# Kernel tuning notes

Measured on AMD Instinct MI355X. Metric: run time of the kernel, lower is better.

Reference implementation:

```python
import jax, jax.numpy as jnp
import numpy as np

B = 1024
IN_SIZ = 16384
OUT_SIZ = 16384
C = 8          # channel_siz
NLVL = 10
IFS = IN_SIZ // 2 ** NLVL                                   # 16, in_filter_siz
KLVL = min(int(np.floor(np.log2(OUT_SIZ / 2))), NLVL)       # 10
OFS = OUT_SIZ // 2 ** KLVL                                  # 16, out_filter_siz
STD = 0.9


def setup_inputs() -> dict:
    key = jax.random.key(0)
    ks = jax.random.split(key, 2 * NLVL + 3)
    inp = {}
    inp["x"] = jax.random.normal(ks[0], (B, IN_SIZ, 1), jnp.float32)
    inp["in_filter"] = jax.random.normal(ks[1], (IFS, 1, C), jnp.float32) * STD
    inp["in_bias"] = jnp.zeros((C,), jnp.float32)
    for lvl in range(1, NLVL + 1):
        k = 2 ** lvl
        inp[f"W{lvl}"] = jax.random.normal(ks[2 * lvl], (k, 2, C, C), jnp.float32) * STD
        inp[f"b{lvl}"] = jnp.zeros((k, C), jnp.float32)
    inp["fea_dense"] = jax.random.normal(ks[-1], (2 ** KLVL, C, OFS), jnp.float32) * STD
    return inp


def _level(v, W, b):
    # v: [Kp, B, L, C] parent branches; W: [2*Kp, 2, C, C]; b: [2*Kp, C]
    # kernel-2 stride-2 conv1d: out[t] = relu(x[2t] @ W[0] + x[2t+1] @ W[1] + b)
    Kp, Bn, L, Cc = v.shape
    xp = v.reshape(Kp, Bn, L // 2, 2, Cc)
    xr = jnp.repeat(xp, 2, axis=0)  # child itk reads parent itk // 2
    y = jnp.einsum('kbtsc,kscd->kbtd', xr, W) + b[:, None, None, :]
    return jax.nn.relu(y)


def reference(x, in_filter, in_bias,
              W1, b1, W2, b2, W3, b3, W4, b4, W5, b5,
              W6, b6, W7, b7, W8, b8, W9, b9, W10, b10,
              fea_dense):
    Ws = [W1, W2, W3, W4, W5, W6, W7, W8, W9, W10]
    bs = [b1, b2, b3, b4, b5, b6, b7, b8, b9, b10]
    Bn = x.shape[0]
    # input conv1d: kernel=IFS, stride=IFS (non-overlapping) == blocked matmul
    xin = x[..., 0].reshape(Bn, 2 ** NLVL, IFS)                       # [B, 1024, 16]
    v = jax.nn.relu(jnp.einsum('bnf,fc->bnc', xin, in_filter[:, 0, :]) + in_bias)
    v = v[None]                                                        # [1, B, 1024, C]
    for lvl in range(NLVL):  # klvl == nlvl: all levels branch (tree doubling)
        v = _level(v, Ws[lvl], bs[lvl])
    # v: [2^klvl, B, 1, C] -> per-branch dense feature map
    out = jnp.einsum('kbc,kcf->bkf', v[:, :, 0, :], fea_dense)         # [B, 1024, OFS]
    return out.reshape(Bn, OUT_SIZ, 1)
```

## Files before the change

kernel.cpp:

```cpp
#include <hip/hip_runtime.h>

struct PrepPtrs {
  const float* W[7]; const float* Bv[7]; const float* F; const float* fb;
  const float* W8; const float* B8; const float* W9; const float* B9;
  const float* W10; const float* B10;
};

__device__ __forceinline__ int cz(int c) { return c ^ ((c >> 3) & 3); }

__device__ __forceinline__ float4 relu4(float4 a) {
  return make_float4(fmaxf(a.x,0.f), fmaxf(a.y,0.f), fmaxf(a.z,0.f), fmaxf(a.w,0.f));
}
__device__ __forceinline__ void fma4(float4& acc, float s, const float4& wv) {
  acc.x = fmaf(s, wv.x, acc.x); acc.y = fmaf(s, wv.y, acc.y);
  acc.z = fmaf(s, wv.z, acc.z); acc.w = fmaf(s, wv.w, acc.w);
}
__device__ __forceinline__ float4 add4(float4 a, float4 b) {
  return make_float4(a.x+b.x, a.y+b.y, a.z+b.z, a.w+b.w);
}

__device__ __forceinline__ float4 entApply(const float4* __restrict__ e4,
                                           float4 A0, float4 A1,
                                           float4 C0, float4 C1) {
  float4 a0 = e4[16];
  float4 a1 = make_float4(0.f, 0.f, 0.f, 0.f);
  float4 a2 = make_float4(0.f, 0.f, 0.f, 0.f);
  float4 a3 = make_float4(0.f, 0.f, 0.f, 0.f);
  fma4(a0, A0.x, e4[0]);  fma4(a1, A0.y, e4[1]);  fma4(a2, A0.z, e4[2]);  fma4(a3, A0.w, e4[3]);
  fma4(a0, A1.x, e4[4]);  fma4(a1, A1.y, e4[5]);  fma4(a2, A1.z, e4[6]);  fma4(a3, A1.w, e4[7]);
  fma4(a0, C0.x, e4[8]);  fma4(a1, C0.y, e4[9]);  fma4(a2, C0.z, e4[10]); fma4(a3, C0.w, e4[11]);
  fma4(a0, C1.x, e4[12]); fma4(a1, C1.y, e4[13]); fma4(a2, C1.z, e4[14]); fma4(a3, C1.w, e4[15]);
  return relu4(add4(add4(a0, a1), add4(a2, a3)));
}

__global__ void bfly_prep(PrepPtrs P, float* __restrict__ wt) {
  int e = blockIdx.x * 256 + threadIdx.x;
  if (e >= 4094 * 68) return;
  int ent = e / 68, r = e % 68, dd = r & 3;
  const float* Ws; const float* Bs; int th;
  if (ent < 62) {
    if (ent < 60) {
      int lvl, base;
      if (ent < 4)       { lvl = 1; base = 0;  }
      else if (ent < 12) { lvl = 2; base = 4;  }
      else if (ent < 28) { lvl = 3; base = 12; }
      else               { lvl = 4; base = 28; }
      int k = (ent - base) >> 1; th = ent & 1;
      Ws = P.W[lvl-1] + k*128; Bs = P.Bv[lvl-1] + k*8;
    } else {
      th = ent - 60; Ws = P.F; Bs = P.fb;
    }
  } else if (ent < 510) {
    int eb = ent - 62;
    int q = eb / 56, rem = eb % 56;
    int lvl, Kl, base;
    if (rem < 8)       { lvl = 5; Kl = 4;  base = 0;  }
    else if (rem < 24) { lvl = 6; Kl = 8;  base = 8;  }
    else               { lvl = 7; Kl = 16; base = 24; }
    int rr = rem - base; int lk = rr >> 1; th = rr & 1;
    int kg = q * Kl + lk;
    Ws = P.W[lvl-1] + kg*128; Bs = P.Bv[lvl-1] + kg*8;
  } else if (ent < 1022) {
    int ec = ent - 510; int k = ec >> 1; th = ec & 1;
    Ws = P.W8 + k*128; Bs = P.B8 + k*8;
  } else if (ent < 2046) {
    int ec = ent - 1022; int k = ec >> 1; th = ec & 1;
    Ws = P.W9 + k*128; Bs = P.B9 + k*8;
  } else {
    int ec = ent - 2046; int k = ec >> 1; th = ec & 1;
    Ws = P.W10 + k*128; Bs = P.B10 + k*8;
  }
  float v;
  if (r < 64) { int s = r >> 5, c = (r >> 2) & 7; v = Ws[s*64 + c*8 + th*4 + dd]; }
  else v = Bs[th*4 + dd];
  wt[ent * 80 + r] = v;
}

template<int L>
__device__ __forceinline__ void ka_level(const float4* __restrict__ src,
                                         float4* __restrict__ dst,
                                         const float4* __restrict__ wt4,
                                         int lane, int wq, int th) {
  constexpr int Kc = 1 << L, Tc = 1024 >> L;
  constexpr int entBase = (Kc - 2) * 2;
  constexpr int kIters = (L <= 2) ? 1 : (1 << (L - 2));
  constexpr int tIters = 4 / kIters;
#pragma unroll
  for (int ik = 0; ik < kIters; ++ik) {
    int k;
    if constexpr (L == 1) k = wq & 1;
    else if constexpr (L == 2) k = wq;
    else k = wq + 4 * ik;
    const float4* e4 = wt4 + (entBase + k * 2 + th) * 20;
    const int kp = k >> 1;
#pragma unroll
    for (int it = 0; it < tIters; ++it) {
      int t;
      if constexpr (L == 1) t = lane + (wq >> 1) * 64 + it * 128;
      else if constexpr (L == 2) t = lane + it * 64;
      else if constexpr (L == 3) t = lane + it * 64;
      else t = lane;
      int pb = kp * (2 * Tc) + 2 * t;
      float4 A0 = src[cz(pb)],        C0 = src[cz(pb + 1)];
      float4 A1 = src[cz(pb + 1024)], C1 = src[cz(pb + 1025)];
      dst[cz(th * 1024 + k * Tc + t)] = entApply(e4, A0, A1, C0, C1);
    }
  }
}

__global__ __launch_bounds__(512, 2) void bfly_ka(
    const float* __restrict__ x, const float* __restrict__ wt,
    float* __restrict__ st1)
{
  __shared__ float4 sA[2048], sB[2048];
  const int tid = threadIdx.x, b = blockIdx.x;
  const int lane = tid & 63;
  const int wv = __builtin_amdgcn_readfirstlane(tid >> 6);
  const int th = wv & 1, wq = wv >> 1;
  const float4* wt4 = (const float4*)wt;

  {
    const float4* e4 = wt4 + (60 + th) * 20;
    const float* xb = x + (size_t)b * 16384;
#pragma unroll
    for (int i = 0; i < 4; ++i) {
      int n = lane + wq * 64 + i * 256;
      const float4* xr = (const float4*)(xb + n * 16);
      float4 x0 = xr[0], x1 = xr[1], x2 = xr[2], x3 = xr[3];
      sA[cz(th * 1024 + n)] = entApply(e4, x0, x1, x2, x3);
    }
  }
  __syncthreads();
  ka_level<1>(sA, sB, wt4, lane, wq, th); __syncthreads();
  ka_level<2>(sB, sA, wt4, lane, wq, th); __syncthreads();
  ka_level<3>(sA, sB, wt4, lane, wq, th); __syncthreads();
  ka_level<4>(sB, sA, wt4, lane, wq, th); __syncthreads();

  float4* o4 = (float4*)st1;
#pragma unroll
  for (int it = 0; it < 4; ++it) {
    int o = tid + it * 512;
    int t4 = o & 63, k4 = (o >> 6) & 15, h = o >> 10;
    o4[((size_t)(h * 16 + k4) * 1024 + b) * 64 + t4] = sA[cz(o)];
  }
}

template<int LV>
__device__ __forceinline__ void kb_level(const float4* __restrict__ src,
                                         float4* __restrict__ dst,
                                         const float4* __restrict__ wb4,
                                         int lane, int wv) {
  constexpr int Kc = 1 << (LV - 3);
  constexpr int Tc = 128 / Kc;
  constexpr int Tp = 256 / Kc;
  constexpr int entB = (LV == 5) ? 0 : (LV == 6) ? 8 : 24;
  constexpr int kIters = Kc / 4;
  constexpr int nIt = 4 / kIters;
  const int th = wv & 1, w2 = wv >> 1;
#pragma unroll
  for (int ik = 0; ik < kIters; ++ik) {
    const int lk = w2 + 4 * ik;
    const float4* e4 = wb4 + (entB + lk * 2 + th) * 20;
    const int lkp = lk >> 1;
#pragma unroll
    for (int it = 0; it < nIt; ++it) {
      int t, bb;
      if constexpr (LV == 5)      { t = lane & 31; bb = (lane >> 5) + it * 2; }
      else if constexpr (LV == 6) { t = lane & 15; bb = (lane >> 4) + it * 4; }
      else                        { t = lane & 7;  bb = lane >> 3; }
      int pb = bb * 256 + lkp * Tp + 2 * t;
      float4 A0 = src[cz(pb)],       C0 = src[cz(pb + 1)];
      float4 A1 = src[cz(pb + 128)], C1 = src[cz(pb + 129)];
      dst[cz(bb * 256 + th * 128 + lk * Tc + t)] = entApply(e4, A0, A1, C0, C1);
    }
  }
}

__global__ __launch_bounds__(512, 2) void bfly_kb(
    const float* __restrict__ st1, const float* __restrict__ wt,
    float* __restrict__ st2)
{
  __shared__ float4 s0[2048], s1[2048];
  const int tid = threadIdx.x;
  const int q = blockIdx.x, bt = blockIdx.y;
  const int lane = tid & 63;
  const int wv = __builtin_amdgcn_readfirstlane(tid >> 6);
  const float4* wb4 = (const float4*)wt + 1240 + q * 56 * 20;
  const float4* i4 = (const float4*)st1;

#pragma unroll
  for (int it = 0; it < 4; ++it) {
    int o = tid + it * 512;
    int t4 = o & 63, lk4 = (o >> 6) & 1, h = (o >> 7) & 1, bl = o >> 8;
    float4 v = i4[((size_t)(h * 16 + 2 * q + lk4) * 1024 + bt * 8 + bl) * 64 + t4];
    s0[cz(bl * 256 + h * 128 + lk4 * 64 + t4)] = v;
  }
  __syncthreads();
  kb_level<5>(s0, s1, wb4, lane, wv); __syncthreads();
  kb_level<6>(s1, s0, wb4, lane, wv); __syncthreads();
  kb_level<7>(s0, s1, wb4, lane, wv); __syncthreads();

  float4* o4 = (float4*)st2;
#pragma unroll
  for (int it = 0; it < 4; ++it) {
    int o = tid + it * 512;
    int bl = o & 7, t7 = (o >> 3) & 7, h = (o >> 6) & 1, lk7 = o >> 7;
    float4 v = s1[cz(bl * 256 + h * 128 + lk7 * 8 + t7)];
    o4[((size_t)((16 * q + lk7) * 8 + t7) * 2 + h) * 1024 + bt * 8 + bl] = v;
  }
}

__global__ __launch_bounds__(512, 2) void bfly_kc(
    const float* __restrict__ st, const float* __restrict__ wt,
    const float* __restrict__ fea, float* __restrict__ out)
{
  __shared__ float4 sA[1024], sB[1024];
  const int tid = threadIdx.x;
  const int j = blockIdx.x, b0 = blockIdx.y * 64;
  const int bb = tid & 63;
  const int w = __builtin_amdgcn_readfirstlane(tid >> 6);
  const float4* wt4 = (const float4*)wt;

  {
    const float4* s4 = (const float4*)st;
#pragma unroll
    for (int it = 0; it < 2; ++it) {
      int idx = tid + it * 512;
      int bl = idx & 63, h = (idx >> 6) & 1, t = idx >> 7;
      sA[h * 512 + t * 64 + bl] = s4[((size_t)((j * 8 + t) * 2 + h)) * 1024 + b0 + bl];
    }
  }
  __syncthreads();

#pragma unroll
  for (int ii = 0; ii < 2; ++ii) {
    int s = w + ii * 8;
    int th = s >> 3, k = (s >> 2) & 1, t = s & 3;
    const float4* e4 = wt4 + (510 + (2 * j + k) * 2 + th) * 20;
    float4 A0 = sA[(2*t) * 64 + bb],   A1 = sA[512 + (2*t) * 64 + bb];
    float4 C0 = sA[(2*t+1) * 64 + bb], C1 = sA[512 + (2*t+1) * 64 + bb];
    sB[th * 512 + (2*t + k) * 64 + bb] = entApply(e4, A0, A1, C0, C1);
  }
  __syncthreads();
#pragma unroll
  for (int ii = 0; ii < 2; ++ii) {
    int s = w + ii * 8;
    int th = s >> 3, k9 = (s >> 1) & 3, t9 = s & 1;
    const float4* e4 = wt4 + (1022 + (4 * j + k9) * 2 + th) * 20;
    int p0 = 4 * t9 + (k9 >> 1), p1 = p0 + 2;
    float4 A0 = sB[p0 * 64 + bb], A1 = sB[512 + p0 * 64 + bb];
    float4 C0 = sB[p1 * 64 + bb], C1 = sB[512 + p1 * 64 + bb];
    sA[th * 512 + (t9 * 4 + k9) * 64 + bb] = entApply(e4, A0, A1, C0, C1);
  }
  __syncthreads();
#pragma unroll
  for (int ii = 0; ii < 2; ++ii) {
    int s = w + ii * 8;
    int th = s >> 3, k10 = s & 7;
    const float4* e4 = wt4 + (2046 + (8 * j + k10) * 2 + th) * 20;
    int p0 = k10 >> 1, p1 = p0 + 4;
    float4 A0 = sA[p0 * 64 + bb], A1 = sA[512 + p0 * 64 + bb];
    float4 C0 = sA[p1 * 64 + bb], C1 = sA[512 + p1 * 64 + bb];
    sB[th * 512 + k10 * 64 + bb] = entApply(e4, A0, A1, C0, C1);
  }
  __syncthreads();
  {
    int cc = tid & 31, bgrp = tid >> 5;
    int k = cc >> 2, fq = cc & 3;
    const float* fp = fea + (size_t)(j * 8 + k) * 128 + fq * 4;
    float4 f0 = *(const float4*)(fp);        float4 f1 = *(const float4*)(fp + 16);
    float4 f2 = *(const float4*)(fp + 32);   float4 f3 = *(const float4*)(fp + 48);
    float4 f4_ = *(const float4*)(fp + 64);  float4 f5 = *(const float4*)(fp + 80);
    float4 f6 = *(const float4*)(fp + 96);   float4 f7 = *(const float4*)(fp + 112);
#pragma unroll
    for (int it = 0; it < 4; ++it) {
      int b_l = bgrp + it * 16;
      float4 s0v = sB[k * 64 + b_l];
      float4 s1v = sB[512 + k * 64 + b_l];
      float4 a0 = make_float4(0.f,0.f,0.f,0.f), a1 = make_float4(0.f,0.f,0.f,0.f);
      float4 a2 = make_float4(0.f,0.f,0.f,0.f), a3 = make_float4(0.f,0.f,0.f,0.f);
      fma4(a0, s0v.x, f0);  fma4(a1, s0v.y, f1);
      fma4(a2, s0v.z, f2);  fma4(a3, s0v.w, f3);
      fma4(a0, s1v.x, f4_); fma4(a1, s1v.y, f5);
      fma4(a2, s1v.z, f6);  fma4(a3, s1v.w, f7);
      float4 acc = add4(add4(a0, a1), add4(a2, a3));
      *(float4*)(out + ((size_t)(b0 + b_l)) * 16384 + j * 128 + k * 16 + fq * 4) = acc;
    }
  }
}

extern "C" void kernel_launch(void* const* d_in, const int* in_sizes, int n_in,
                              void* d_out, int out_size, void* d_ws, size_t ws_size,
                              hipStream_t stream) {
  const float* x  = (const float*)d_in[0];
  PrepPtrs P;
  P.F  = (const float*)d_in[1];
  P.fb = (const float*)d_in[2];
  for (int l = 0; l < 7; ++l) {
    P.W[l]  = (const float*)d_in[3 + 2 * l];
    P.Bv[l] = (const float*)d_in[4 + 2 * l];
  }
  P.W8  = (const float*)d_in[17];
  P.B8  = (const float*)d_in[18];
  P.W9  = (const float*)d_in[19];
  P.B9  = (const float*)d_in[20];
  P.W10 = (const float*)d_in[21];
  P.B10 = (const float*)d_in[22];
  const float* fea = (const float*)d_in[23];
  float* wt  = (float*)d_ws;
  float* st2 = (float*)d_ws + 393216;
  float* st1 = (float*)d_out;
  float* out = (float*)d_out;

  bfly_prep<<<dim3(1088), dim3(256), 0, stream>>>(P, wt);
  bfly_ka<<<dim3(1024), dim3(512), 0, stream>>>(x, wt, st1);
  bfly_kb<<<dim3(8, 128), dim3(512), 0, stream>>>(st1, wt, st2);
  bfly_kc<<<dim3(128, 16), dim3(512), 0, stream>>>(st2, wt, fea, out);
}
```

Baseline: 95.83 us.

## Compute all four children per thread from one parent load; make kb in-place

Each butterfly level now has a thread load its parent pair once into registers and produce all four child outputs (two child branches by two output halves), instead of reloading the same inputs for each child. This cuts shared-memory reads per level by about four times. bfly_kb now works in place in a single LDS buffer, which halves its shared memory and lets launch_bounds allow three blocks per CU. In-place updates are only safe because each (batch, parent) region is read and written by the same wavefront. The cost is higher register pressure, since each thread holds four outputs' worth of work.

```diff
diff --git a/kernel.cpp b/kernel.cpp
--- a/kernel.cpp
+++ b/kernel.cpp
@@ -77,35 +77,29 @@
 }
 
 template<int L>
-__device__ __forceinline__ void ka_level(const float4* __restrict__ src,
-                                         float4* __restrict__ dst,
-                                         const float4* __restrict__ wt4,
-                                         int lane, int wq, int th) {
-  constexpr int Kc = 1 << L, Tc = 1024 >> L;
-  constexpr int entBase = (Kc - 2) * 2;
-  constexpr int kIters = (L <= 2) ? 1 : (1 << (L - 2));
-  constexpr int tIters = 4 / kIters;
-#pragma unroll
-  for (int ik = 0; ik < kIters; ++ik) {
-    int k;
-    if constexpr (L == 1) k = wq & 1;
-    else if constexpr (L == 2) k = wq;
-    else k = wq + 4 * ik;
-    const float4* e4 = wt4 + (entBase + k * 2 + th) * 20;
-    const int kp = k >> 1;
-#pragma unroll
-    for (int it = 0; it < tIters; ++it) {
-      int t;
-      if constexpr (L == 1) t = lane + (wq >> 1) * 64 + it * 128;
-      else if constexpr (L == 2) t = lane + it * 64;
-      else if constexpr (L == 3) t = lane + it * 64;
-      else t = lane;
-      int pb = kp * (2 * Tc) + 2 * t;
-      float4 A0 = src[cz(pb)],        C0 = src[cz(pb + 1)];
-      float4 A1 = src[cz(pb + 1024)], C1 = src[cz(pb + 1025)];
-      dst[cz(th * 1024 + k * Tc + t)] = entApply(e4, A0, A1, C0, C1);
-    }
-  }
+__device__ __forceinline__ void ka_level2(const float4* __restrict__ src,
+                                          float4* __restrict__ dst,
+                                          const float4* __restrict__ wt4,
+                                          int lane, int w) {
+  constexpr int Tc = 1024 >> L;
+  constexpr int entBase = ((1 << L) - 2) * 2;
+  constexpr int TB = 1 << (4 - L);
+  const int kp = w >> (4 - L);
+  const int tb = w & (TB - 1);
+  const int t = lane + tb * 64;
+  const int pb = kp * (2 * Tc) + 2 * t;
+  const int cb = cz(pb);
+  const int cb1 = cb ^ 1;
+  float4 A0 = src[cb],        C0 = src[cb1];
+  float4 A1 = src[cb + 1024], C1 = src[cb1 + 1024];
+  float4* pD = dst + cz(2 * kp * Tc + t);
+#pragma unroll
+  for (int kk = 0; kk < 2; ++kk)
+#pragma unroll
+    for (int th = 0; th < 2; ++th) {
+      const float4* e4 = wt4 + (entBase + (2 * kp + kk) * 2 + th) * 20;
+      pD[kk * Tc + th * 1024] = entApply(e4, A0, A1, C0, C1);
+    }
 }
 
 __global__ __launch_bounds__(512, 2) void bfly_ka(
@@ -115,8 +109,8 @@
   __shared__ float4 sA[2048], sB[2048];
   const int tid = threadIdx.x, b = blockIdx.x;
   const int lane = tid & 63;
-  const int wv = __builtin_amdgcn_readfirstlane(tid >> 6);
-  const int th = wv & 1, wq = wv >> 1;
+  const int w = __builtin_amdgcn_readfirstlane(tid >> 6);
+  const int th = w & 1, wq = w >> 1;
   const float4* wt4 = (const float4*)wt;
 
   {
@@ -131,10 +125,10 @@
     }
   }
   __syncthreads();
-  ka_level<1>(sA, sB, wt4, lane, wq, th); __syncthreads();
-  ka_level<2>(sB, sA, wt4, lane, wq, th); __syncthreads();
-  ka_level<3>(sA, sB, wt4, lane, wq, th); __syncthreads();
-  ka_level<4>(sB, sA, wt4, lane, wq, th); __syncthreads();
+  ka_level2<1>(sA, sB, wt4, lane, w); __syncthreads();
+  ka_level2<2>(sB, sA, wt4, lane, w); __syncthreads();
+  ka_level2<3>(sA, sB, wt4, lane, w); __syncthreads();
+  ka_level2<4>(sB, sA, wt4, lane, w); __syncthreads();
 
   float4* o4 = (float4*)st1;
 #pragma unroll
@@ -146,45 +140,40 @@
 }
 
 template<int LV>
-__device__ __forceinline__ void kb_level(const float4* __restrict__ src,
-                                         float4* __restrict__ dst,
-                                         const float4* __restrict__ wb4,
-                                         int lane, int wv) {
-  constexpr int Kc = 1 << (LV - 3);
-  constexpr int Tc = 128 / Kc;
-  constexpr int Tp = 256 / Kc;
+__device__ __forceinline__ void kb_level2(float4* __restrict__ s,
+                                          const float4* __restrict__ wb4,
+                                          int lane, int w) {
+  constexpr int Tc = 1 << (10 - LV);
   constexpr int entB = (LV == 5) ? 0 : (LV == 6) ? 8 : 24;
-  constexpr int kIters = Kc / 4;
-  constexpr int nIt = 4 / kIters;
-  const int th = wv & 1, w2 = wv >> 1;
-#pragma unroll
-  for (int ik = 0; ik < kIters; ++ik) {
-    const int lk = w2 + 4 * ik;
-    const float4* e4 = wb4 + (entB + lk * 2 + th) * 20;
-    const int lkp = lk >> 1;
-#pragma unroll
-    for (int it = 0; it < nIt; ++it) {
-      int t, bb;
-      if constexpr (LV == 5)      { t = lane & 31; bb = (lane >> 5) + it * 2; }
-      else if constexpr (LV == 6) { t = lane & 15; bb = (lane >> 4) + it * 4; }
-      else                        { t = lane & 7;  bb = lane >> 3; }
-      int pb = bb * 256 + lkp * Tp + 2 * t;
-      float4 A0 = src[cz(pb)],       C0 = src[cz(pb + 1)];
-      float4 A1 = src[cz(pb + 128)], C1 = src[cz(pb + 129)];
-      dst[cz(bb * 256 + th * 128 + lk * Tc + t)] = entApply(e4, A0, A1, C0, C1);
-    }
-  }
-}
-
-__global__ __launch_bounds__(512, 2) void bfly_kb(
+  int kp, bl, t;
+  if constexpr (LV == 5)      { kp = w >> 2; bl = ((w & 3) << 1) | (lane >> 5); t = lane & 31; }
+  else if constexpr (LV == 6) { kp = w >> 1; bl = ((w & 1) << 2) | (lane >> 4); t = lane & 15; }
+  else                        { kp = w;      bl = lane >> 3;                    t = lane & 7;  }
+  const int pb = bl * 256 + kp * (2 * Tc) + 2 * t;
+  const int cb = cz(pb);
+  const int cb1 = cb ^ 1;
+  float4 A0 = s[cb],       C0 = s[cb1];
+  float4 A1 = s[cb + 128], C1 = s[cb1 + 128];
+#pragma unroll
+  for (int kk = 0; kk < 2; ++kk) {
+    float4* pD = s + cz(bl * 256 + (2 * kp + kk) * Tc + t);
+#pragma unroll
+    for (int th = 0; th < 2; ++th) {
+      const float4* e4 = wb4 + (entB + (2 * kp + kk) * 2 + th) * 20;
+      pD[th * 128] = entApply(e4, A0, A1, C0, C1);
+    }
+  }
+}
+
+__global__ __launch_bounds__(512, 3) void bfly_kb(
     const float* __restrict__ st1, const float* __restrict__ wt,
     float* __restrict__ st2)
 {
-  __shared__ float4 s0[2048], s1[2048];
+  __shared__ float4 s0[2048];
   const int tid = threadIdx.x;
   const int q = blockIdx.x, bt = blockIdx.y;
   const int lane = tid & 63;
-  const int wv = __builtin_amdgcn_readfirstlane(tid >> 6);
+  const int w = __builtin_amdgcn_readfirstlane(tid >> 6);
   const float4* wb4 = (const float4*)wt + 1240 + q * 56 * 20;
   const float4* i4 = (const float4*)st1;
 
@@ -196,16 +185,16 @@
     s0[cz(bl * 256 + h * 128 + lk4 * 64 + t4)] = v;
   }
   __syncthreads();
-  kb_level<5>(s0, s1, wb4, lane, wv); __syncthreads();
-  kb_level<6>(s1, s0, wb4, lane, wv); __syncthreads();
-  kb_level<7>(s0, s1, wb4, lane, wv); __syncthreads();
+  kb_level2<5>(s0, wb4, lane, w); __syncthreads();
+  kb_level2<6>(s0, wb4, lane, w); __syncthreads();
+  kb_level2<7>(s0, wb4, lane, w); __syncthreads();
 
   float4* o4 = (float4*)st2;
 #pragma unroll
   for (int it = 0; it < 4; ++it) {
     int o = tid + it * 512;
     int bl = o & 7, t7 = (o >> 3) & 7, h = (o >> 6) & 1, lk7 = o >> 7;
-    float4 v = s1[cz(bl * 256 + h * 128 + lk7 * 8 + t7)];
+    float4 v = s0[cz(bl * 256 + h * 128 + lk7 * 8 + t7)];
     o4[((size_t)((16 * q + lk7) * 8 + t7) * 2 + h) * 1024 + bt * 8 + bl] = v;
   }
 }
```

Result: slower. 100.5 us (+4.9%).
